# Optimization experiments

Measured on AMD Instinct MI355X. Metric: run time of the kernel, lower is better.

## Reference

```python
import jax, jax.numpy as jnp
import numpy as np

B_, N_, D_ = 8, 1024, 64
H_, DH_ = 4, 16
DI_, DS_, DTR_ = 128, 64, 4
MAXP = 512


def _ln(x, w, b, eps=1e-5):
    m = jnp.mean(x, -1, keepdims=True)
    v = jnp.mean((x - m) ** 2, -1, keepdims=True)
    return (x - m) * jax.lax.rsqrt(v + eps) * w + b


def _attn(x, drop_mask, Wq, Wkv, Wo, bo, rel_emb):
    b, n, d = x.shape
    scale = DH_ ** -0.5
    q = (x @ Wq).reshape(b, n, H_, DH_).transpose(0, 2, 1, 3)
    kv = x @ Wkv
    k = kv[..., :d].reshape(b, n, H_, DH_).transpose(0, 2, 1, 3)
    v = kv[..., d:].reshape(b, n, H_, DH_).transpose(0, 2, 1, 3)
    dots = jnp.einsum('bhid,bhjd->bhij', q, k) * scale
    seq = jnp.arange(n)
    dist = jnp.clip(seq[:, None] - seq[None, :], -MAXP, MAXP) + MAXP
    rpe = rel_emb[dist]  # (n, n, DH_)
    dots = dots + jnp.einsum('bhid,ijd->bhij', q, rpe) * scale
    # stochastic key drop: Bernoulli(0.3) positions get -1e12
    dots = dots + drop_mask.astype(dots.dtype) * (-1e12)
    attn = jax.nn.softmax(dots, axis=-1)
    out = jnp.einsum('bhij,bhjd->bhid', attn, v)
    out = out.transpose(0, 2, 1, 3).reshape(b, n, H_ * DH_)
    return out @ Wo + bo


def _mamba(x, W_in, conv_w, conv_b, W_xproj, W_dt, b_dt, A_log, Dm, W_out):
    b, n, _ = x.shape
    xz = x @ W_in                      # (b, n, 2*DI_)
    u, z = xz[..., :DI_], xz[..., DI_:]
    uc = u.transpose(0, 2, 1)          # (b, DI_, n)
    uc = jax.lax.conv_general_dilated(
        uc, conv_w[:, None, :], (1,), ((3, 0),),
        feature_group_count=DI_, dimension_numbers=('NCH', 'OIH', 'NCH'))
    uc = uc + conv_b[None, :, None]
    u = jax.nn.silu(uc).transpose(0, 2, 1)  # (b, n, DI_)
    xdb = u @ W_xproj                  # (b, n, DTR_+2*DS_)
    dt = jax.nn.softplus(xdb[..., :DTR_] @ W_dt + b_dt)  # (b, n, DI_)
    Bm = xdb[..., DTR_:DTR_ + DS_]
    Cm = xdb[..., DTR_ + DS_:]
    A = -jnp.exp(A_log)                # (DI_, DS_)

    def step(h, inp):
        dt_t, B_t, C_t, u_t = inp      # (b,DI_),(b,DS_),(b,DS_),(b,DI_)
        dA = jnp.exp(dt_t[..., None] * A)
        h = h * dA + (dt_t * u_t)[..., None] * B_t[:, None, :]
        y = jnp.einsum('bds,bs->bd', h, C_t)
        return h, y

    h0 = jnp.zeros((b, DI_, DS_), x.dtype)
    xs = (dt.transpose(1, 0, 2), Bm.transpose(1, 0, 2),
          Cm.transpose(1, 0, 2), u.transpose(1, 0, 2))
    _, ys = jax.lax.scan(step, h0, xs)
    y = ys.transpose(1, 0, 2) + u * Dm
    y = y * jax.nn.silu(z)
    return y @ W_out


def _rmsgn(x, gamma, eps=1e-5, groups=4):
    shp = x.shape
    dpg = shp[-1] // groups
    xg = x.reshape(shp[:-1] + (groups, dpg))
    rms = jnp.sqrt(jnp.sum(xg * xg, -1, keepdims=True)) * (dpg ** -0.5)
    return (xg / (rms + eps)).reshape(shp) * gamma


def _ff1(x, c1_w, c1_b, d1_w, d1_b):
    # SwiGLUConvDeconv1d(64, 256, kernel=4, shift=1); x: (b, s2, 64)
    s2 = x.shape[1]
    xc = x.transpose(0, 2, 1)
    xc = jnp.pad(xc, ((0, 0), (0, 0), (3, 3)))
    xc = jax.lax.conv_general_dilated(
        xc, c1_w, (1,), 'VALID', dimension_numbers=('NCH', 'OIH', 'NCH'))
    xc = xc + c1_b[None, :, None]
    gate = jax.nn.silu(xc[:, 256:, :])
    xc = xc[:, :256, :] * gate
    # ConvTranspose1d stride 1 == conv with flipped kernel, full padding
    w = jnp.flip(d1_w, -1).transpose(1, 0, 2)  # (64, 256, 4)
    xc = jax.lax.conv_general_dilated(
        xc, w, (1,), ((3, 3),), dimension_numbers=('NCH', 'OIH', 'NCH'))
    xc = xc + d1_b[None, :, None]
    out = xc.transpose(0, 2, 1)
    return out[:, 3:3 + s2, :]


def _forward(x, drop_mask, ln1_w, ln1_b, Wq, Wkv, Wo, bo, rel_emb,
             ln2_w, ln2_b, W_in, conv_w, conv_b, W_xproj, W_dt, b_dt,
             A_log, Dm, W_out, gamma, c1_w, c1_b, d1_w, d1_b, ln3_w, ln3_b):
    xt = _ln(x, ln1_w, ln1_b)
    xt = _attn(xt, drop_mask, Wq, Wkv, Wo, bo, rel_emb) + x
    x = x + xt  # dropout p=0 -> identity (faithful to original residual math)
    xt = _ln(x, ln2_w, ln2_b)
    m = _mamba(xt, W_in, conv_w, conv_b, W_xproj, W_dt, b_dt, A_log, Dm, W_out)
    m = jnp.where(m >= 0, m, 0.01 * m)  # leaky_relu
    m = _rmsgn(m, gamma)
    m = m + 0.5 * _ff1(m, c1_w, c1_b, d1_w, d1_b)
    x = x + m
    return _ln(x, ln3_w, ln3_b)


def setup_inputs() -> dict:
    ks = jax.random.split(jax.random.key(0), 16)
    g = lambda i, shp, s: jax.random.normal(ks[i], shp, dtype=jnp.float32) * s
    A_log = jnp.log(jnp.tile(jnp.arange(1, DS_ + 1, dtype=jnp.float32)[None, :], (DI_, 1)))
    return {
        'x': jax.random.normal(ks[0], (B_, N_, D_), dtype=jnp.float32),
        'drop_mask': jax.random.bernoulli(ks[1], 0.3, (B_, H_, N_, N_)),
        'ln1_w': jnp.ones((D_,), jnp.float32), 'ln1_b': jnp.zeros((D_,), jnp.float32),
        'Wq': g(2, (D_, D_), 0.1), 'Wkv': g(3, (D_, 2 * D_), 0.1),
        'Wo': g(4, (D_, D_), 0.1), 'bo': jnp.zeros((D_,), jnp.float32),
        'rel_emb': g(5, (2 * MAXP + 1, DH_), 0.02),
        'ln2_w': jnp.ones((D_,), jnp.float32), 'ln2_b': jnp.zeros((D_,), jnp.float32),
        'W_in': g(6, (D_, 2 * DI_), 0.1),
        'conv_w': g(7, (DI_, 4), 0.2), 'conv_b': jnp.zeros((DI_,), jnp.float32),
        'W_xproj': g(8, (DI_, DTR_ + 2 * DS_), 0.1),
        'W_dt': g(9, (DTR_, DI_), 0.1), 'b_dt': jnp.zeros((DI_,), jnp.float32),
        'A_log': A_log, 'Dm': jnp.ones((DI_,), jnp.float32),
        'W_out': g(10, (DI_, D_), 0.1),
        'gamma': jnp.ones((D_,), jnp.float32),
        'c1_w': g(11, (512, 64, 4), 0.1), 'c1_b': jnp.zeros((512,), jnp.float32),
        'd1_w': g(12, (256, 64, 4), 0.1), 'd1_b': jnp.zeros((64,), jnp.float32),
        'ln3_w': jnp.ones((D_,), jnp.float32), 'ln3_b': jnp.zeros((D_,), jnp.float32),
    }


def reference(x, drop_mask, ln1_w, ln1_b, Wq, Wkv, Wo, bo, rel_emb,
              ln2_w, ln2_b, W_in, conv_w, conv_b, W_xproj, W_dt, b_dt,
              A_log, Dm, W_out, gamma, c1_w, c1_b, d1_w, d1_b, ln3_w, ln3_b):
    return _forward(x, drop_mask, ln1_w, ln1_b, Wq, Wkv, Wo, bo, rel_emb,
                    ln2_w, ln2_b, W_in, conv_w, conv_b, W_xproj, W_dt, b_dt,
                    A_log, Dm, W_out, gamma, c1_w, c1_b, d1_w, d1_b, ln3_w, ln3_b)
```

## Files before the change

### kernel.cpp

```cpp
#include <hip/hip_runtime.h>
#include <hip/hip_fp16.h>
#include <math.h>


__device__ __forceinline__ float wsum64(float v){
#pragma unroll
  for(int m=32;m>0;m>>=1) v += __shfl_xor(v, m, 64);
  return v;
}
__device__ __forceinline__ float wmax64(float v){
#pragma unroll
  for(int m=32;m>0;m>>=1) v = fmaxf(v, __shfl_xor(v, m, 64));
  return v;
}
__device__ __forceinline__ float silu_f(float x){ return x / (1.f + __expf(-x)); }

__global__ __launch_bounds__(256) void k_ln1_qkv(
    const float* __restrict__ x, const float* __restrict__ w1, const float* __restrict__ b1,
    const float* __restrict__ Wq, const float* __restrict__ Wkv,
    const float* __restrict__ rel, const float* __restrict__ c1w,
    float* __restrict__ qb, float2* __restrict__ kvT,
    float* __restrict__ relT, float* __restrict__ c1wT){
  int lane = threadIdx.x & 63, warp = threadIdx.x >> 6;
  int token = blockIdx.x*4 + warp;
  __shared__ float xt[4][64];
  float xv = x[(size_t)token*64 + lane];
  float mean = wsum64(xv) * 0.015625f;
  float dlt = xv - mean;
  float var = wsum64(dlt*dlt) * 0.015625f;
  float xn = dlt * rsqrtf(var + 1e-5f) * w1[lane] + b1[lane];
  xt[warp][lane] = xn;
  __syncthreads();
  float aq=0.f, ak=0.f, av=0.f;
#pragma unroll 4
  for(int dd=0; dd<64; ++dd){
    float xd = xt[warp][dd];
    aq += xd * Wq[dd*64 + lane];
    ak += xd * Wkv[dd*128 + lane];
    av += xd * Wkv[dd*128 + 64 + lane];
  }
  int b = token >> 10, i = token & 1023;
  int h = lane >> 4, dh = lane & 15;
  size_t o  = (((size_t)(b*4 + h))*1024 + i)*16 + dh;
  size_t oT = (((size_t)(b*4 + h))*16 + dh)*1024 + i;
  qb[o]=aq;
  kvT[oT] = make_float2(ak, av);

  if (blockIdx.x < 65){
    int idx = blockIdx.x*256 + threadIdx.x;
    if (idx < 16*1025){
      int c = idx / 1025;
      int d = idx - c*1025;
      relT[idx] = rel[d*16 + c];
    }
  } else if (blockIdx.x < 577){
    int idx = (blockIdx.x-65)*256 + threadIdx.x;
    int row = idx >> 9;
    int ii  = idx & 511;
    c1wT[idx] = c1w[(size_t)ii*256 + row];
  }
}

__global__ __launch_bounds__(256) void k_kmax(
    const float2* __restrict__ kvT, float* __restrict__ Kmax){
  int bh = blockIdx.x; int tid = threadIdx.x;
  const float2* base = kvT + (size_t)bh*16*1024;
  float mx = 0.f;
#pragma unroll
  for(int r=0;r<4;++r){
    int j = tid + 256*r;
    float ss = 0.f;
#pragma unroll
    for(int c=0;c<16;++c){ float2 kv = base[c*1024 + j]; ss += kv.x*kv.x; }
    mx = fmaxf(mx, ss);
  }
  mx = wmax64(mx);
  __shared__ float red[4];
  int lane = tid&63, wv = tid>>6;
  if(lane==0) red[wv]=mx;
  __syncthreads();
  if(tid==0) Kmax[bh] = sqrtf(fmaxf(fmaxf(red[0],red[1]),fmaxf(red[2],red[3])));
}

__global__ __launch_bounds__(256, 3) void k_attn(
    const float* __restrict__ qb, const float2* __restrict__ kvT,
    const int* __restrict__ dmask, const float* __restrict__ relT,
    const float* __restrict__ Kmax, float* __restrict__ attn_raw){
  int tid = threadIdx.x;
  int lane = tid & 63, wv = tid >> 6;
  int bh  = blockIdx.y;
  int i0  = blockIdx.x*8;
  int b = bh >> 2, h = bh & 3;
  int r0 = wv*2, r1 = wv*2 + 1;

  __shared__ __half Gc[8][1024];
  __shared__ float red[8*272];
  __shared__ float qs[8][16];
  __shared__ float G0s[8], G1024s[8];
  __shared__ float gmS[8];
  __shared__ float Ms[8];
  __shared__ float sums[8];

  if (tid < 128){
    int r = tid >> 4, c = tid & 15;
    qs[r][c] = qb[((size_t)bh*1024 + i0 + r)*16 + c] * 0.25f;
  }
  __syncthreads();

#pragma unroll 1
  for(int bb=0; bb<5; ++bb){
    int d = tid + 256*bb;
    if (d <= 1024){
      float rl[16];
#pragma unroll
      for(int c=0;c<16;++c) rl[c] = relT[c*1025 + d];
#pragma unroll
      for(int r=0;r<8;++r){
        float g = 0.f;
#pragma unroll
        for(int c=0;c<16;++c) g += qs[r][c]*rl[c];
        if (d == 0)        G0s[r] = g;
        else if (d == 1024) G1024s[r] = g;
        else {
          int j = i0 + r + 512 - d;
          if (j >= 0 && j < 1024) Gc[r][j] = __float2half(g);
        }
      }
    }
  }
  __syncthreads();
#pragma unroll
  for(int r=0;r<8;++r){
    __half g0 = __float2half(G0s[r]), g1 = __float2half(G1024s[r]);
    int lo = i0 + r - 512;
    int hi = i0 + r + 512;
#pragma unroll
    for(int p=0;p<4;++p){
      int j = tid + 256*p;
      if (j >= hi) Gc[r][j] = g0;
      else if (j <= lo) Gc[r][j] = g1;
    }
  }
  __syncthreads();
  {
    int r = tid >> 5, jb = tid & 31;
    float gm = -3.0e38f;
#pragma unroll
    for(int k=0;k<32;++k) gm = fmaxf(gm, __half2float(Gc[r][jb + 32*k]));
#pragma unroll
    for(int m=1;m<32;m<<=1) gm = fmaxf(gm, __shfl_xor(gm, m, 64));
    if ((lane&31)==0) gmS[r] = gm;
  }
  __syncthreads();
  if (tid < 8){
    float qn = 0.f;
#pragma unroll
    for(int c=0;c<16;++c) qn += qs[tid][c]*qs[tid][c];
    Ms[tid] = gmS[tid] + sqrtf(qn)*Kmax[bh];
  }
  __syncthreads();

  float q0[16], q1[16];
#pragma unroll
  for(int c=0;c<16;++c){ q0[c]=qs[r0][c]; q1[c]=qs[r1][c]; }
  float M0 = Ms[r0], M1 = Ms[r1];

  const float2* kvb = kvT + (size_t)bh*16*1024;
  const int* mb0 = dmask + ((size_t)bh*1024 + i0 + r0)*1024;
  const int* mb1 = dmask + ((size_t)bh*1024 + i0 + r1)*1024;

  float s0=0.f, s1=0.f;
  float a0[16], a1[16];
#pragma unroll
  for(int c=0;c<16;++c){ a0[c]=0.f; a1[c]=0.f; }

#pragma unroll 1
  for(int t=0;t<16;++t){
    int j = lane + 64*t;
    int mk0 = mb0[j], mk1 = mb1[j];
    float2 kv[16];
#pragma unroll
    for(int c=0;c<16;++c) kv[c] = kvb[c*1024 + j];
    float sv0 = __half2float(Gc[r0][j]), sv1 = __half2float(Gc[r1][j]);
#pragma unroll
    for(int c=0;c<16;++c){ sv0 += q0[c]*kv[c].x; sv1 += q1[c]*kv[c].x; }
    float p0 = mk0 ? 0.f : __expf(sv0 - M0);
    float p1 = mk1 ? 0.f : __expf(sv1 - M1);
    s0 += p0; s1 += p1;
#pragma unroll
    for(int c=0;c<16;++c){ a0[c] += p0*kv[c].y; a1[c] += p1*kv[c].y; }
  }
  s0 = wsum64(s0); s1 = wsum64(s1);
#pragma unroll
  for(int c=0;c<16;++c){
    float x0 = a0[c];
    x0 += __shfl_xor(x0, 32, 64); x0 += __shfl_xor(x0, 16, 64);
    a0[c] = x0;
    float x1 = a1[c];
    x1 += __shfl_xor(x1, 32, 64); x1 += __shfl_xor(x1, 16, 64);
    a1[c] = x1;
  }
  if (lane < 16){
#pragma unroll
    for(int c=0;c<16;++c){
      red[r0*272 + lane*17 + c] = a0[c];
      red[r1*272 + lane*17 + c] = a1[c];
    }
  }
  if (lane == 0){ sums[r0] = s0; sums[r1] = s1; }
  __syncthreads();
  if (tid < 128){
    int row = tid >> 4, c = tid & 15;
    float tot = 0.f;
#pragma unroll
    for(int g=0; g<16; ++g) tot += red[row*272 + g*17 + c];
    attn_raw[((size_t)b*1024 + i0 + row)*64 + h*16 + c] = tot / sums[row];
  }
}

__global__ __launch_bounds__(256) void k_post_attn(
    const float* __restrict__ x, const float* __restrict__ attn_raw,
    const float* __restrict__ Wo, const float* __restrict__ bo,
    const float* __restrict__ ln2w, const float* __restrict__ ln2b,
    const float* __restrict__ W_in,
    float* __restrict__ x2, float* __restrict__ u0, float* __restrict__ zsarr){
  int tid = threadIdx.x;
  int lane = tid & 63, wv = tid >> 6;
  int tok0 = blockIdx.x * 16;
  __shared__ float arS[16][64];
  __shared__ float lnS[16][64];
  for(int l = tid; l < 1024; l += 256)
    arS[l >> 6][l & 63] = attn_raw[(size_t)tok0*64 + l];
  __syncthreads();
#pragma unroll 1
  for(int tt = 0; tt < 4; ++tt){
    int tl = wv*4 + tt;
    int token = tok0 + tl;
    float acc = bo[lane];
#pragma unroll 4
    for(int dd = 0; dd < 64; ++dd) acc += arS[tl][dd] * Wo[dd*64 + lane];
    float t = 2.f*x[(size_t)token*64 + lane] + acc;
    x2[(size_t)token*64 + lane] = t;
    float mean = wsum64(t)*0.015625f;
    float dlt = t - mean;
    float var = wsum64(dlt*dlt)*0.015625f;
    lnS[tl][lane] = dlt*rsqrtf(var+1e-5f)*ln2w[lane] + ln2b[lane];
  }
  __syncthreads();
  int oc = tid;
  float w[64];
#pragma unroll
  for(int dd = 0; dd < 64; ++dd) w[dd] = W_in[dd*256 + oc];
  const float4* lnS4 = (const float4*)&lnS[0][0];
#pragma unroll 1
  for(int tl = 0; tl < 16; ++tl){
    float acc = 0.f;
#pragma unroll
    for(int d4 = 0; d4 < 16; ++d4){
      float4 l4 = lnS4[tl*16 + d4];
      acc += l4.x*w[4*d4] + l4.y*w[4*d4+1] + l4.z*w[4*d4+2] + l4.w*w[4*d4+3];
    }
    int token = tok0 + tl;
    if (oc < 128) u0[(size_t)token*128 + oc] = acc;
    else          zsarr[(size_t)token*128 + (oc-128)] = silu_f(acc);
  }
}

__global__ __launch_bounds__(256) void k_conv_proj(
    const float* __restrict__ u0, const float* __restrict__ conv_w, const float* __restrict__ conv_b,
    const float* __restrict__ W_xproj, const float* __restrict__ W_dt, const float* __restrict__ b_dt,
    float* __restrict__ uarr, float* __restrict__ Bmp, float* __restrict__ Cmp, float* __restrict__ dtarr){
  int tid = threadIdx.x;
  int tok0 = blockIdx.x * 16;
  int b = tok0 >> 10, i0 = tok0 & 1023;
  __shared__ float u0S[19][128];
  __shared__ float usS[16][128];
  __shared__ float dtin[16][4];
  for(int l = tid; l < 19*128; l += 256){
    int row = l >> 7, c = l & 127;
    int t = i0 - 3 + row;
    u0S[row][c] = (t >= 0) ? u0[((size_t)b*1024 + t)*128 + c] : 0.f;
  }
  __syncthreads();
#pragma unroll
  for(int pp=0; pp<8; ++pp){
    int p = tid + 256*pp;
    int tl = p >> 7, c = p & 127;
    float acc = conv_b[c];
#pragma unroll
    for(int k2=0;k2<4;++k2) acc += u0S[tl+k2][c]*conv_w[c*4+k2];
    float uv = silu_f(acc);
    usS[tl][c] = uv;
    uarr[(size_t)(tok0+tl)*128 + c] = uv;
  }
  __syncthreads();
  int sub = tid >> 7, c = tid & 127;
  int cB = 128 + (c & 3);
  float accA[8], accB[8];
#pragma unroll
  for(int tt=0;tt<8;++tt){ accA[tt]=0.f; accB[tt]=0.f; }
#pragma unroll 2
  for(int dd=0; dd<128; ++dd){
    float wA = W_xproj[dd*132 + c];
    float wB = W_xproj[dd*132 + cB];
#pragma unroll
    for(int tt=0;tt<8;++tt){
      float xd = usS[sub*8+tt][dd];
      accA[tt] += xd*wA; accB[tt] += xd*wB;
    }
  }
#pragma unroll
  for(int tt=0;tt<8;++tt){
    int tl = sub*8 + tt;
    int token = tok0 + tl;
    if (c < 4){ dtin[tl][c] = accA[tt]; Cmp[(size_t)token*64 + 60 + c] = accB[tt]; }
    else if (c < 68) Bmp[(size_t)token*64 + (c-4)] = accA[tt];
    else             Cmp[(size_t)token*64 + (c-68)] = accA[tt];
  }
  __syncthreads();
#pragma unroll
  for(int pp=0;pp<8;++pp){
    int p = tid + 256*pp;
    int tl = p >> 7, c2 = p & 127;
    float dv = b_dt[c2];
#pragma unroll
    for(int r2=0;r2<4;++r2) dv += dtin[tl][r2]*W_dt[r2*128 + c2];
    dv = fmaxf(dv, 0.f) + log1pf(expf(-fabsf(dv)));
    dtarr[(size_t)(tok0+tl)*128 + c2] = dv;
  }
}

__global__ __launch_bounds__(256) void k_scan_a(
    const float* __restrict__ dtarr, const float* __restrict__ uarr,
    const float* __restrict__ Bmp, const float* __restrict__ A_log,
    float* __restrict__ Parr, float* __restrict__ Rarr){
  int lane = threadIdx.x & 63, warp = threadIdx.x >> 6;
  int w = blockIdx.x*4 + warp;
  int c = w & 7, d = (w >> 3) & 127, b = w >> 10;
  float A = -expf(A_log[d*64 + lane]);
  int tb = c*128;
  const float* dtp = dtarr + ((size_t)b*1024 + tb)*128 + d;
  const float* up  = uarr  + ((size_t)b*1024 + tb)*128 + d;
  const float* Bp  = Bmp   + ((size_t)b*1024 + tb)*64 + lane;
  float R = 0.f, sdt = 0.f;
  for(int t0=0; t0<128; t0+=8){
    float dtc[8], uc[8], Bc[8];
#pragma unroll
    for(int r=0;r<8;++r){
      dtc[r]=dtp[(size_t)(t0+r)*128]; uc[r]=up[(size_t)(t0+r)*128]; Bc[r]=Bp[(size_t)(t0+r)*64];
    }
#pragma unroll
    for(int r=0;r<8;++r){
      float dt = dtc[r];
      R = R*__expf(dt*A) + dt*uc[r]*Bc[r];
      sdt += dt;
    }
  }
  Parr[(size_t)w*64 + lane] = __expf(sdt*A);
  Rarr[(size_t)w*64 + lane] = R;
}

__global__ __launch_bounds__(256) void k_scan_c(
    const float* __restrict__ dtarr, const float* __restrict__ uarr,
    const float* __restrict__ Bmp, const float* __restrict__ Cmp,
    const float* __restrict__ zsarr, const float* __restrict__ A_log,
    const float* __restrict__ Dm, const float* __restrict__ Parr,
    const float* __restrict__ Rarr, float* __restrict__ ymp){
  int lane = threadIdx.x & 63, warp = threadIdx.x >> 6;
  int w = blockIdx.x*4 + warp;
  int c = w & 7, d = (w >> 3) & 127, b = w >> 10;
  float A = -expf(A_log[d*64 + lane]);
  float Dv = Dm[d];
  float h = 0.f;
  int wbase = w - c;
#pragma unroll 1
  for(int cp=0; cp<c; ++cp){
    float P = Parr[(size_t)(wbase+cp)*64 + lane];
    float R = Rarr[(size_t)(wbase+cp)*64 + lane];
    h = h*P + R;
  }
  int tb = c*128;
  const float* dtp = dtarr + ((size_t)b*1024 + tb)*128 + d;
  const float* up  = uarr  + ((size_t)b*1024 + tb)*128 + d;
  const float* zp  = zsarr + ((size_t)b*1024 + tb)*128 + d;
  const float* Bp  = Bmp   + ((size_t)b*1024 + tb)*64 + lane;
  const float* Cp  = Cmp   + ((size_t)b*1024 + tb)*64 + lane;
  float* yp        = ymp   + ((size_t)b*1024 + tb)*128 + d;
  for(int t0=0; t0<128; t0+=8){
    float dtc[8], uc[8], Bc[8], Cc[8], zc[8];
#pragma unroll
    for(int r=0;r<8;++r){
      dtc[r]=dtp[(size_t)(t0+r)*128]; uc[r]=up[(size_t)(t0+r)*128];
      Bc[r]=Bp[(size_t)(t0+r)*64];    Cc[r]=Cp[(size_t)(t0+r)*64];
      zc[r]=zp[(size_t)(t0+r)*128];
    }
    float hc[8];
#pragma unroll
    for(int r=0;r<8;++r){
      float dt = dtc[r];
      h = h*__expf(dt*A) + dt*uc[r]*Bc[r];
      hc[r] = h*Cc[r];
    }
    float y[8];
#pragma unroll
    for(int r=0;r<8;++r) y[r] = wsum64(hc[r]);
    if (lane==0){
#pragma unroll
      for(int r=0;r<8;++r) yp[(size_t)(t0+r)*128] = (y[r] + uc[r]*Dv)*zc[r];
    }
  }
}

__global__ __launch_bounds__(256) void k_wout(
    const float* __restrict__ ymp, const float* __restrict__ W_out,
    const float* __restrict__ gamma, float* __restrict__ marr){
  int tid = threadIdx.x;
  int lane = tid & 63, wv = tid >> 6;
  int tok0 = blockIdx.x * 16;
  __shared__ float ysS[16][128];
  for(int l = tid; l < 16*128; l += 256)
    ysS[l >> 7][l & 127] = ymp[(size_t)tok0*128 + l];
  __syncthreads();
  float acc[4];
#pragma unroll
  for(int tt=0;tt<4;++tt) acc[tt]=0.f;
#pragma unroll 2
  for(int dd=0; dd<128; ++dd){
    float w = W_out[dd*64 + lane];
#pragma unroll
    for(int tt=0;tt<4;++tt) acc[tt] += ysS[wv*4+tt][dd]*w;
  }
  float g = gamma[lane];
#pragma unroll
  for(int tt=0;tt<4;++tt){
    float a = acc[tt];
    a = a >= 0.f ? a : 0.01f*a;
    float ss = a*a;
#pragma unroll
    for(int m=1;m<16;m<<=1) ss += __shfl_xor(ss, m, 64);
    float rms = sqrtf(ss)*0.25f;
    marr[(size_t)(tok0 + wv*4 + tt)*64 + lane] = a/(rms + 1e-5f)*g;
  }
}

__global__ __launch_bounds__(256) void k_h2(
    const float* __restrict__ marr, const float* __restrict__ c1wT,
    const float* __restrict__ c1b, float* __restrict__ h2){
  int b = blockIdx.y;
  int t0 = blockIdx.x * 16;
  int tid = threadIdx.x;
  __shared__ float ms[19][64];
  for(int l = tid; l < 19*64; l += 256){
    int row = l >> 6, cc = l & 63;
    int t = t0 - 3 + row;
    ms[row][cc] = (t >= 0 && t < 1024) ? marr[((size_t)b*1024 + t)*64 + cc] : 0.f;
  }
  __syncthreads();
  int i = tid;
  float acc1[16], acc2[16];
#pragma unroll
  for(int tl=0;tl<16;++tl){ acc1[tl]=0.f; acc2[tl]=0.f; }
  for(int cc=0; cc<64; ++cc){
    float mv[19];
#pragma unroll
    for(int r2=0;r2<19;++r2) mv[r2] = ms[r2][cc];
    const float* wr = c1wT + (size_t)cc*4*512;
    float wa0 = wr[      i], wa1 = wr[ 512+i], wa2 = wr[1024+i], wa3 = wr[1536+i];
    float wg0 = wr[  256+i], wg1 = wr[ 768+i], wg2 = wr[1280+i], wg3 = wr[1792+i];
#pragma unroll
    for(int tl=0; tl<16; ++tl){
      acc1[tl] += wa0*mv[tl+0] + wa1*mv[tl+1] + wa2*mv[tl+2] + wa3*mv[tl+3];
      acc2[tl] += wg0*mv[tl+0] + wg1*mv[tl+1] + wg2*mv[tl+2] + wg3*mv[tl+3];
    }
  }
  float bb1 = c1b[i], bb2 = c1b[i+256];
#pragma unroll
  for(int tl=0; tl<16; ++tl){
    int t = t0 + tl;
    if (t < 1027){
      float o1 = acc1[tl] + bb1;
      float o2 = acc2[tl] + bb2;
      h2[((size_t)b*1027 + t)*256 + i] = o1 * silu_f(o2);
    }
  }
}

__global__ __launch_bounds__(256) void k_ff_final(
    const float* __restrict__ h2, const float* __restrict__ d1w, const float* __restrict__ d1b,
    const float* __restrict__ x2, const float* __restrict__ marr,
    const float* __restrict__ ln3w, const float* __restrict__ ln3b,
    float* __restrict__ out){
  int b = blockIdx.y;
  int s0 = blockIdx.x * 16;
  int tid = threadIdx.x;
  int o = tid & 63, sg = tid >> 6;
  __shared__ float hs[19][256];
  for(int l = tid; l < 19*256; l += 256){
    int row = l >> 8, cc = l & 255;
    hs[row][cc] = h2[((size_t)b*1027 + s0 + row)*256 + cc];
  }
  __syncthreads();
  int sl = sg*4;
  float acc0=0.f, acc1=0.f, acc2=0.f, acc3=0.f;
  const float4* wb = (const float4*)d1w + o;
#pragma unroll 2
  for(int i2=0; i2<256; ++i2){
    float4 wv = wb[(size_t)i2*64];
    float h0=hs[sl+0][i2], h1=hs[sl+1][i2], h2v=hs[sl+2][i2], h3=hs[sl+3][i2];
    float h4=hs[sl+4][i2], h5=hs[sl+5][i2], h6=hs[sl+6][i2];
    acc0 += h0*wv.w + h1*wv.z + h2v*wv.y + h3*wv.x;
    acc1 += h1*wv.w + h2v*wv.z + h3*wv.y + h4*wv.x;
    acc2 += h2v*wv.w + h3*wv.z + h4*wv.y + h5*wv.x;
    acc3 += h3*wv.w + h4*wv.z + h5*wv.y + h6*wv.x;
  }
  float accs[4] = {acc0, acc1, acc2, acc3};
  float bo_ = d1b[o];
#pragma unroll
  for(int r=0;r<4;++r){
    int s = s0 + sl + r;
    size_t idx = ((size_t)b*1024 + s)*64 + o;
    float tot = x2[idx] + marr[idx] + 0.5f*(accs[r] + bo_);
    float mean = wsum64(tot)*0.015625f;
    float dlt = tot - mean;
    float var = wsum64(dlt*dlt)*0.015625f;
    out[idx] = dlt*rsqrtf(var+1e-5f)*ln3w[o] + ln3b[o];
  }
}

extern "C" void kernel_launch(void* const* d_in, const int* in_sizes, int n_in,
                              void* d_out, int out_size, void* d_ws, size_t ws_size,
                              hipStream_t stream){
  const float* x       = (const float*)d_in[0];
  const int*   dmask   = (const int*)  d_in[1];
  const float* ln1w    = (const float*)d_in[2];
  const float* ln1b    = (const float*)d_in[3];
  const float* Wq      = (const float*)d_in[4];
  const float* Wkv     = (const float*)d_in[5];
  const float* Wo      = (const float*)d_in[6];
  const float* bo      = (const float*)d_in[7];
  const float* rel     = (const float*)d_in[8];
  const float* ln2w    = (const float*)d_in[9];
  const float* ln2b    = (const float*)d_in[10];
  const float* W_in    = (const float*)d_in[11];
  const float* conv_w  = (const float*)d_in[12];
  const float* conv_b  = (const float*)d_in[13];
  const float* W_xproj = (const float*)d_in[14];
  const float* W_dt    = (const float*)d_in[15];
  const float* b_dt    = (const float*)d_in[16];
  const float* A_log   = (const float*)d_in[17];
  const float* Dm      = (const float*)d_in[18];
  const float* W_out   = (const float*)d_in[19];
  const float* gamma   = (const float*)d_in[20];
  const float* c1w     = (const float*)d_in[21];
  const float* c1b     = (const float*)d_in[22];
  const float* d1w     = (const float*)d_in[23];
  const float* d1b     = (const float*)d_in[24];
  const float* ln3w    = (const float*)d_in[25];
  const float* ln3b    = (const float*)d_in[26];
  float* outp = (float*)d_out;

  float* ws = (float*)d_ws;
  float* qb       = ws;
  float* kvT      = qb      + 524288;
  float* attn_raw = kvT     + 1048576;
  float* x2       = attn_raw+ 524288;
  float* u0       = x2      + 524288;
  float* zsarr    = u0      + 1048576;
  float* uarr     = zsarr   + 1048576;
  float* dtarr    = uarr    + 1048576;
  float* Bmp      = dtarr   + 1048576;
  float* Cmp      = Bmp     + 524288;
  float* ymp      = Cmp     + 524288;
  float* marr     = ymp     + 1048576;
  float* h2       = marr    + 524288;
  float* relT     = h2      + 2103296;
  float* c1wT     = relT    + 16400;
  float* Parr     = c1wT    + 131072;
  float* Rarr     = Parr    + 524288;
  float* Kmaxa    = Rarr    + 524288;

  k_ln1_qkv  <<<2048, 256, 0, stream>>>(x, ln1w, ln1b, Wq, Wkv, rel, c1w,
                                        qb, (float2*)kvT, relT, c1wT);
  k_kmax     <<<32, 256, 0, stream>>>((const float2*)kvT, Kmaxa);
  k_attn     <<<dim3(128,32), 256, 0, stream>>>(qb, (const float2*)kvT, dmask, relT, Kmaxa, attn_raw);
  k_post_attn<<<512, 256, 0, stream>>>(x, attn_raw, Wo, bo, ln2w, ln2b, W_in, x2, u0, zsarr);
  k_conv_proj<<<512, 256, 0, stream>>>(u0, conv_w, conv_b, W_xproj, W_dt, b_dt, uarr, Bmp, Cmp, dtarr);
  k_scan_a   <<<2048, 256, 0, stream>>>(dtarr, uarr, Bmp, A_log, Parr, Rarr);
  k_scan_c   <<<2048, 256, 0, stream>>>(dtarr, uarr, Bmp, Cmp, zsarr, A_log, Dm, Parr, Rarr, ymp);
  k_wout     <<<512, 256, 0, stream>>>(ymp, W_out, gamma, marr);
  k_h2       <<<dim3(65,8), 256, 0, stream>>>(marr, c1wT, c1b, h2);
  k_ff_final <<<dim3(64,8), 256, 0, stream>>>(h2, d1w, d1b, x2, marr, ln3w, ln3b, outp);
}
```

Baseline: 756.3 us.

## Fuse Kmax into QKV, merge post-attn with conv, merge scan passes

Computes the per-head key-norm max inside the QKV kernel using atomicMax on float bits over a zeroed buffer, which removes the separate k_kmax launch. Fuses post-attention projection, LN2 and W_in into the conv/xproj kernel. Each block recomputes 3 halo tokens so the u0 round-trip through global memory is no longer needed. Merges the two-pass chunked scan into one 512-thread block per (batch, channel), with chunk prefix states exchanged through shared memory instead of the Parr/Rarr global arrays. This reduces launches and global traffic in exchange for redundant halo compute and atomics.

```diff
diff --git a/kernel.cpp b/kernel.cpp
--- a/kernel.cpp
+++ b/kernel.cpp
@@ -20,10 +20,12 @@
     const float* __restrict__ Wq, const float* __restrict__ Wkv,
     const float* __restrict__ rel, const float* __restrict__ c1w,
     float* __restrict__ qb, float2* __restrict__ kvT,
-    float* __restrict__ relT, float* __restrict__ c1wT){
+    float* __restrict__ relT, float* __restrict__ c1wT,
+    float* __restrict__ Kmax2){
   int lane = threadIdx.x & 63, warp = threadIdx.x >> 6;
   int token = blockIdx.x*4 + warp;
   __shared__ float xt[4][64];
+  __shared__ float knS[4][4];
   float xv = x[(size_t)token*64 + lane];
   float mean = wsum64(xv) * 0.015625f;
   float dlt = xv - mean;
@@ -46,6 +48,17 @@
   qb[o]=aq;
   kvT[oT] = make_float2(ak, av);
 
+  float kn = ak*ak;
+  kn += __shfl_xor(kn,1,64); kn += __shfl_xor(kn,2,64);
+  kn += __shfl_xor(kn,4,64); kn += __shfl_xor(kn,8,64);
+  if (dh == 0) knS[warp][h] = kn;
+  __syncthreads();
+  if (threadIdx.x < 4){
+    float m = fmaxf(fmaxf(knS[0][threadIdx.x],knS[1][threadIdx.x]),
+                    fmaxf(knS[2][threadIdx.x],knS[3][threadIdx.x]));
+    atomicMax((int*)&Kmax2[b*4 + threadIdx.x], __float_as_int(m));
+  }
+
   if (blockIdx.x < 65){
     int idx = blockIdx.x*256 + threadIdx.x;
     if (idx < 16*1025){
@@ -61,31 +74,10 @@
   }
 }
 
-__global__ __launch_bounds__(256) void k_kmax(
-    const float2* __restrict__ kvT, float* __restrict__ Kmax){
-  int bh = blockIdx.x; int tid = threadIdx.x;
-  const float2* base = kvT + (size_t)bh*16*1024;
-  float mx = 0.f;
-#pragma unroll
-  for(int r=0;r<4;++r){
-    int j = tid + 256*r;
-    float ss = 0.f;
-#pragma unroll
-    for(int c=0;c<16;++c){ float2 kv = base[c*1024 + j]; ss += kv.x*kv.x; }
-    mx = fmaxf(mx, ss);
-  }
-  mx = wmax64(mx);
-  __shared__ float red[4];
-  int lane = tid&63, wv = tid>>6;
-  if(lane==0) red[wv]=mx;
-  __syncthreads();
-  if(tid==0) Kmax[bh] = sqrtf(fmaxf(fmaxf(red[0],red[1]),fmaxf(red[2],red[3])));
-}
-
 __global__ __launch_bounds__(256, 3) void k_attn(
     const float* __restrict__ qb, const float2* __restrict__ kvT,
     const int* __restrict__ dmask, const float* __restrict__ relT,
-    const float* __restrict__ Kmax, float* __restrict__ attn_raw){
+    const float* __restrict__ Kmax2, float* __restrict__ attn_raw){
   int tid = threadIdx.x;
   int lane = tid & 63, wv = tid >> 6;
   int bh  = blockIdx.y;
@@ -156,7 +148,7 @@
     float qn = 0.f;
 #pragma unroll
     for(int c=0;c<16;++c) qn += qs[tid][c]*qs[tid][c];
-    Ms[tid] = gmS[tid] + sqrtf(qn)*Kmax[bh];
+    Ms[tid] = gmS[tid] + sqrtf(qn)*sqrtf(Kmax2[bh]);
   }
   __syncthreads();
 
@@ -218,68 +210,66 @@
   }
 }
 
-__global__ __launch_bounds__(256) void k_post_attn(
+__global__ __launch_bounds__(256) void k_postattn_conv(
     const float* __restrict__ x, const float* __restrict__ attn_raw,
     const float* __restrict__ Wo, const float* __restrict__ bo,
     const float* __restrict__ ln2w, const float* __restrict__ ln2b,
     const float* __restrict__ W_in,
-    float* __restrict__ x2, float* __restrict__ u0, float* __restrict__ zsarr){
+    const float* __restrict__ conv_w, const float* __restrict__ conv_b,
+    const float* __restrict__ W_xproj, const float* __restrict__ W_dt, const float* __restrict__ b_dt,
+    float* __restrict__ x2, float* __restrict__ zsarr, float* __restrict__ uarr,
+    float* __restrict__ Bmp, float* __restrict__ Cmp, float* __restrict__ dtarr){
   int tid = threadIdx.x;
   int lane = tid & 63, wv = tid >> 6;
   int tok0 = blockIdx.x * 16;
-  __shared__ float arS[16][64];
-  __shared__ float lnS[16][64];
-  for(int l = tid; l < 1024; l += 256)
-    arS[l >> 6][l & 63] = attn_raw[(size_t)tok0*64 + l];
-  __syncthreads();
-#pragma unroll 1
-  for(int tt = 0; tt < 4; ++tt){
-    int tl = wv*4 + tt;
-    int token = tok0 + tl;
-    float acc = bo[lane];
-#pragma unroll 4
-    for(int dd = 0; dd < 64; ++dd) acc += arS[tl][dd] * Wo[dd*64 + lane];
-    float t = 2.f*x[(size_t)token*64 + lane] + acc;
-    x2[(size_t)token*64 + lane] = t;
-    float mean = wsum64(t)*0.015625f;
-    float dlt = t - mean;
-    float var = wsum64(dlt*dlt)*0.015625f;
-    lnS[tl][lane] = dlt*rsqrtf(var+1e-5f)*ln2w[lane] + ln2b[lane];
-  }
-  __syncthreads();
-  int oc = tid;
-  float w[64];
-#pragma unroll
-  for(int dd = 0; dd < 64; ++dd) w[dd] = W_in[dd*256 + oc];
-  const float4* lnS4 = (const float4*)&lnS[0][0];
-#pragma unroll 1
-  for(int tl = 0; tl < 16; ++tl){
-    float acc = 0.f;
-#pragma unroll
-    for(int d4 = 0; d4 < 16; ++d4){
-      float4 l4 = lnS4[tl*16 + d4];
-      acc += l4.x*w[4*d4] + l4.y*w[4*d4+1] + l4.z*w[4*d4+2] + l4.w*w[4*d4+3];
-    }
-    int token = tok0 + tl;
-    if (oc < 128) u0[(size_t)token*128 + oc] = acc;
-    else          zsarr[(size_t)token*128 + (oc-128)] = silu_f(acc);
-  }
-}
-
-__global__ __launch_bounds__(256) void k_conv_proj(
-    const float* __restrict__ u0, const float* __restrict__ conv_w, const float* __restrict__ conv_b,
-    const float* __restrict__ W_xproj, const float* __restrict__ W_dt, const float* __restrict__ b_dt,
-    float* __restrict__ uarr, float* __restrict__ Bmp, float* __restrict__ Cmp, float* __restrict__ dtarr){
-  int tid = threadIdx.x;
-  int tok0 = blockIdx.x * 16;
   int b = tok0 >> 10, i0 = tok0 & 1023;
+  __shared__ float arS[19][64];
+  __shared__ float lnS[19][64];
   __shared__ float u0S[19][128];
   __shared__ float usS[16][128];
   __shared__ float dtin[16][4];
-  for(int l = tid; l < 19*128; l += 256){
-    int row = l >> 7, c = l & 127;
+  for(int l = tid; l < 19*64; l += 256){
+    int row = l >> 6, cc = l & 63;
     int t = i0 - 3 + row;
-    u0S[row][c] = (t >= 0) ? u0[((size_t)b*1024 + t)*128 + c] : 0.f;
+    arS[row][cc] = (t >= 0) ? attn_raw[((size_t)b*1024 + t)*64 + cc] : 0.f;
+  }
+  __syncthreads();
+#pragma unroll 1
+  for(int k = 0; k < 5; ++k){
+    int row = wv + 4*k;
+    if (row < 19){
+      int t = i0 - 3 + row;
+      float acc = bo[lane];
+#pragma unroll 4
+      for(int dd = 0; dd < 64; ++dd) acc += arS[row][dd] * Wo[dd*64 + lane];
+      float tv = 0.f;
+      if (t >= 0) tv = 2.f*x[((size_t)b*1024 + t)*64 + lane] + acc;
+      if (row >= 3) x2[((size_t)b*1024 + t)*64 + lane] = tv;
+      float mean = wsum64(tv)*0.015625f;
+      float dlt = tv - mean;
+      float var = wsum64(dlt*dlt)*0.015625f;
+      lnS[row][lane] = dlt*rsqrtf(var+1e-5f)*ln2w[lane] + ln2b[lane];
+    }
+  }
+  __syncthreads();
+  {
+    int oc = tid;
+    float w[64];
+#pragma unroll
+    for(int dd = 0; dd < 64; ++dd) w[dd] = W_in[dd*256 + oc];
+    const float4* lnS4 = (const float4*)&lnS[0][0];
+#pragma unroll 1
+    for(int row = 0; row < 19; ++row){
+      float acc = 0.f;
+#pragma unroll
+      for(int d4 = 0; d4 < 16; ++d4){
+        float4 l4 = lnS4[row*16 + d4];
+        acc += l4.x*w[4*d4] + l4.y*w[4*d4+1] + l4.z*w[4*d4+2] + l4.w*w[4*d4+3];
+      }
+      int t = i0 - 3 + row;
+      if (oc < 128) u0S[row][oc] = (t >= 0) ? acc : 0.f;
+      else if (row >= 3) zsarr[(size_t)(tok0 + row - 3)*128 + (oc-128)] = silu_f(acc);
+    }
   }
   __syncthreads();
 #pragma unroll
@@ -294,28 +284,30 @@
     uarr[(size_t)(tok0+tl)*128 + c] = uv;
   }
   __syncthreads();
-  int sub = tid >> 7, c = tid & 127;
-  int cB = 128 + (c & 3);
-  float accA[8], accB[8];
-#pragma unroll
-  for(int tt=0;tt<8;++tt){ accA[tt]=0.f; accB[tt]=0.f; }
+  {
+    int sub = tid >> 7, c = tid & 127;
+    int cB = 128 + (c & 3);
+    float accA[8], accB[8];
+#pragma unroll
+    for(int tt=0;tt<8;++tt){ accA[tt]=0.f; accB[tt]=0.f; }
 #pragma unroll 2
-  for(int dd=0; dd<128; ++dd){
-    float wA = W_xproj[dd*132 + c];
-    float wB = W_xproj[dd*132 + cB];
+    for(int dd=0; dd<128; ++dd){
+      float wA = W_xproj[dd*132 + c];
+      float wB = W_xproj[dd*132 + cB];
+#pragma unroll
+      for(int tt=0;tt<8;++tt){
+        float xd = usS[sub*8+tt][dd];
+        accA[tt] += xd*wA; accB[tt] += xd*wB;
+      }
+    }
 #pragma unroll
     for(int tt=0;tt<8;++tt){
-      float xd = usS[sub*8+tt][dd];
-      accA[tt] += xd*wA; accB[tt] += xd*wB;
-    }
-  }
-#pragma unroll
-  for(int tt=0;tt<8;++tt){
-    int tl = sub*8 + tt;
-    int token = tok0 + tl;
-    if (c < 4){ dtin[tl][c] = accA[tt]; Cmp[(size_t)token*64 + 60 + c] = accB[tt]; }
-    else if (c < 68) Bmp[(size_t)token*64 + (c-4)] = accA[tt];
-    else             Cmp[(size_t)token*64 + (c-68)] = accA[tt];
+      int tl = sub*8 + tt;
+      int token = tok0 + tl;
+      if (c < 4){ dtin[tl][c] = accA[tt]; Cmp[(size_t)token*64 + 60 + c] = accB[tt]; }
+      else if (c < 68) Bmp[(size_t)token*64 + (c-4)] = accA[tt];
+      else             Cmp[(size_t)token*64 + (c-68)] = accA[tt];
+    }
   }
   __syncthreads();
 #pragma unroll
@@ -330,55 +322,17 @@
   }
 }
 
-__global__ __launch_bounds__(256) void k_scan_a(
-    const float* __restrict__ dtarr, const float* __restrict__ uarr,
-    const float* __restrict__ Bmp, const float* __restrict__ A_log,
-    float* __restrict__ Parr, float* __restrict__ Rarr){
-  int lane = threadIdx.x & 63, warp = threadIdx.x >> 6;
-  int w = blockIdx.x*4 + warp;
-  int c = w & 7, d = (w >> 3) & 127, b = w >> 10;
-  float A = -expf(A_log[d*64 + lane]);
-  int tb = c*128;
-  const float* dtp = dtarr + ((size_t)b*1024 + tb)*128 + d;
-  const float* up  = uarr  + ((size_t)b*1024 + tb)*128 + d;
-  const float* Bp  = Bmp   + ((size_t)b*1024 + tb)*64 + lane;
-  float R = 0.f, sdt = 0.f;
-  for(int t0=0; t0<128; t0+=8){
-    float dtc[8], uc[8], Bc[8];
-#pragma unroll
-    for(int r=0;r<8;++r){
-      dtc[r]=dtp[(size_t)(t0+r)*128]; uc[r]=up[(size_t)(t0+r)*128]; Bc[r]=Bp[(size_t)(t0+r)*64];
-    }
-#pragma unroll
-    for(int r=0;r<8;++r){
-      float dt = dtc[r];
-      R = R*__expf(dt*A) + dt*uc[r]*Bc[r];
-      sdt += dt;
-    }
-  }
-  Parr[(size_t)w*64 + lane] = __expf(sdt*A);
-  Rarr[(size_t)w*64 + lane] = R;
-}
-
-__global__ __launch_bounds__(256) void k_scan_c(
+__global__ __launch_bounds__(512) void k_scan(
     const float* __restrict__ dtarr, const float* __restrict__ uarr,
     const float* __restrict__ Bmp, const float* __restrict__ Cmp,
     const float* __restrict__ zsarr, const float* __restrict__ A_log,
-    const float* __restrict__ Dm, const float* __restrict__ Parr,
-    const float* __restrict__ Rarr, float* __restrict__ ymp){
-  int lane = threadIdx.x & 63, warp = threadIdx.x >> 6;
-  int w = blockIdx.x*4 + warp;
-  int c = w & 7, d = (w >> 3) & 127, b = w >> 10;
+    const float* __restrict__ Dm, float* __restrict__ ymp){
+  int tid = threadIdx.x;
+  int lane = tid & 63, c = tid >> 6;
+  int g = blockIdx.x;
+  int b = g >> 7, d = g & 127;
   float A = -expf(A_log[d*64 + lane]);
   float Dv = Dm[d];
-  float h = 0.f;
-  int wbase = w - c;
-#pragma unroll 1
-  for(int cp=0; cp<c; ++cp){
-    float P = Parr[(size_t)(wbase+cp)*64 + lane];
-    float R = Rarr[(size_t)(wbase+cp)*64 + lane];
-    h = h*P + R;
-  }
   int tb = c*128;
   const float* dtp = dtarr + ((size_t)b*1024 + tb)*128 + d;
   const float* up  = uarr  + ((size_t)b*1024 + tb)*128 + d;
@@ -386,6 +340,29 @@
   const float* Bp  = Bmp   + ((size_t)b*1024 + tb)*64 + lane;
   const float* Cp  = Cmp   + ((size_t)b*1024 + tb)*64 + lane;
   float* yp        = ymp   + ((size_t)b*1024 + tb)*128 + d;
+  __shared__ float PS[8][64], RS[8][64];
+  {
+    float R = 0.f, sdt = 0.f;
+    for(int t0=0; t0<128; t0+=8){
+      float dtc[8], uc[8], Bc[8];
+#pragma unroll
+      for(int r=0;r<8;++r){
+        dtc[r]=dtp[(size_t)(t0+r)*128]; uc[r]=up[(size_t)(t0+r)*128]; Bc[r]=Bp[(size_t)(t0+r)*64];
+      }
+#pragma unroll
+      for(int r=0;r<8;++r){
+        float dt = dtc[r];
+        R = R*__expf(dt*A) + dt*uc[r]*Bc[r];
+        sdt += dt;
+      }
+    }
+    PS[c][lane] = __expf(sdt*A);
+    RS[c][lane] = R;
+  }
+  __syncthreads();
+  float h = 0.f;
+#pragma unroll 1
+  for(int cp=0; cp<c; ++cp) h = h*PS[cp][lane] + RS[cp][lane];
   for(int t0=0; t0<128; t0+=8){
     float dtc[8], uc[8], Bc[8], Cc[8], zc[8];
 #pragma unroll
@@ -564,8 +541,7 @@
   float* kvT      = qb      + 524288;
   float* attn_raw = kvT     + 1048576;
   float* x2       = attn_raw+ 524288;
-  float* u0       = x2      + 524288;
-  float* zsarr    = u0      + 1048576;
+  float* zsarr    = x2      + 524288;
   float* uarr     = zsarr   + 1048576;
   float* dtarr    = uarr    + 1048576;
   float* Bmp      = dtarr   + 1048576;
@@ -575,19 +551,17 @@
   float* h2       = marr    + 524288;
   float* relT     = h2      + 2103296;
   float* c1wT     = relT    + 16400;
-  float* Parr     = c1wT    + 131072;
-  float* Rarr     = Parr    + 524288;
-  float* Kmaxa    = Rarr    + 524288;
-
-  k_ln1_qkv  <<<2048, 256, 0, stream>>>(x, ln1w, ln1b, Wq, Wkv, rel, c1w,
-                                        qb, (float2*)kvT, relT, c1wT);
-  k_kmax     <<<32, 256, 0, stream>>>((const float2*)kvT, Kmaxa);
-  k_attn     <<<dim3(128,32), 256, 0, stream>>>(qb, (const float2*)kvT, dmask, relT, Kmaxa, attn_raw);
-  k_post_attn<<<512, 256, 0, stream>>>(x, attn_raw, Wo, bo, ln2w, ln2b, W_in, x2, u0, zsarr);
-  k_conv_proj<<<512, 256, 0, stream>>>(u0, conv_w, conv_b, W_xproj, W_dt, b_dt, uarr, Bmp, Cmp, dtarr);
-  k_scan_a   <<<2048, 256, 0, stream>>>(dtarr, uarr, Bmp, A_log, Parr, Rarr);
-  k_scan_c   <<<2048, 256, 0, stream>>>(dtarr, uarr, Bmp, Cmp, zsarr, A_log, Dm, Parr, Rarr, ymp);
-  k_wout     <<<512, 256, 0, stream>>>(ymp, W_out, gamma, marr);
-  k_h2       <<<dim3(65,8), 256, 0, stream>>>(marr, c1wT, c1b, h2);
-  k_ff_final <<<dim3(64,8), 256, 0, stream>>>(h2, d1w, d1b, x2, marr, ln3w, ln3b, outp);
-}
+  float* Kmaxa    = c1wT    + 131072;
+
+  hipMemsetAsync(Kmaxa, 0, 32*sizeof(float), stream);
+  k_ln1_qkv      <<<2048, 256, 0, stream>>>(x, ln1w, ln1b, Wq, Wkv, rel, c1w,
+                                            qb, (float2*)kvT, relT, c1wT, Kmaxa);
+  k_attn         <<<dim3(128,32), 256, 0, stream>>>(qb, (const float2*)kvT, dmask, relT, Kmaxa, attn_raw);
+  k_postattn_conv<<<512, 256, 0, stream>>>(x, attn_raw, Wo, bo, ln2w, ln2b, W_in,
+                                           conv_w, conv_b, W_xproj, W_dt, b_dt,
+                                           x2, zsarr, uarr, Bmp, Cmp, dtarr);
+  k_scan         <<<1024, 512, 0, stream>>>(dtarr, uarr, Bmp, Cmp, zsarr, A_log, Dm, ymp);
+  k_wout         <<<512, 256, 0, stream>>>(ymp, W_out, gamma, marr);
+  k_h2           <<<dim3(65,8), 256, 0, stream>>>(marr, c1wT, c1b, h2);
+  k_ff_final     <<<dim3(64,8), 256, 0, stream>>>(h2, d1w, d1b, x2, marr, ln3w, ln3b, outp);
+}
```

Result: no change. 743.8 us (-1.7%).
